# Optimization experiments

Hardware: AMD Instinct MI355X
Metric: run time of the kernel (lower is better)

The kernel has to match this reference:

```python
import jax, jax.numpy as jnp
import numpy as np

T, H = 4096, 2048

def setup_inputs() -> dict:
    key = jax.random.key(0)
    k1, k2, k3 = jax.random.split(key, 3)
    x_sequence = jax.random.normal(k1, (T, H), dtype=jnp.float32)
    lamda = jax.random.normal(k2, (H,), dtype=jnp.float32) * 0.2
    B = jax.random.normal(k3, (H, H), dtype=jnp.float32) / jnp.sqrt(jnp.float32(H))
    return {"x_sequence": x_sequence, "lamda": lamda, "B": B}

def reference(x_sequence, lamda, B):
    # h_t = lamda \odot h_{t-1} + B @ x_t ; initial h_0 = 0 (reset_rtrl_state).
    # Returns stacked h over all T steps, matching torch.stack(outputs).
    def step(h, x_t):
        h_next = lamda * h + B @ x_t  # [H]
        return h_next, h_next
    h0 = jnp.zeros_like(lamda)
    _, hs = jax.lax.scan(step, h0, x_sequence)  # hs: [T, H]
    return hs
```

## Files before the change

kernel.cpp:

```cpp
#include <hip/hip_runtime.h>
#include <hip/hip_bf16.h>

#define T_DIM 4096
#define H_DIM 2048
#define K_DIM 2048
#define NCHUNK 64
#define CLEN 64
#define NT (K_DIM / 64)

typedef float f32x4 __attribute__((ext_vector_type(4)));
typedef _Float16 f16x8 __attribute__((ext_vector_type(8)));

typedef const __attribute__((address_space(1))) char* gp1;
typedef __attribute__((address_space(3))) char* lp3;

static const size_t nX = (size_t)T_DIM * K_DIM;
static const size_t nB = (size_t)H_DIM * K_DIM;

__global__ __launch_bounds__(256) void cvt_swz_all(const float* __restrict__ X,
                                                   const float* __restrict__ Bm,
                                                   _Float16* __restrict__ Xh,
                                                   _Float16* __restrict__ Bh) {
    size_t i = ((size_t)blockIdx.x * 256 + threadIdx.x) * 8;
    const float* in;
    _Float16* out;
    size_t j;
    if (i < nX) { in = X;  out = Xh; j = i; }
    else        { in = Bm; out = Bh; j = i - nX; }
    int row  = (int)(j >> 11);
    int colB = (int)(j & 2047) * 2;
    float a[8];
    *(f32x4*)(a)     = *(const f32x4*)(in + j);
    *(f32x4*)(a + 4) = *(const f32x4*)(in + j + 4);
    f16x8 h;
#pragma unroll
    for (int k = 0; k < 8; ++k) h[k] = (_Float16)a[k];
    size_t ob = (size_t)row * 4096 + (size_t)(colB ^ ((row & 7) << 4));
    *(f16x8*)((char*)out + ob) = h;
}

__global__ __launch_bounds__(256) void gemm_f16(const _Float16* __restrict__ Xh,
                                                const _Float16* __restrict__ Bh,
                                                const float* __restrict__ lamda,
                                                float* __restrict__ Y,
                                                float* __restrict__ e) {
    __shared__ __align__(16) _Float16 sA[2][128 * 64];
    __shared__ __align__(16) _Float16 sB[2][128 * 64];

    int bid = blockIdx.x;
    int swz = (bid & 7) * 64 + (bid >> 3);
    const int h0 = (swz & 15) * 128;
    const int t0 = (swz >> 4) * 128;

    const int tid  = threadIdx.x;
    const int lane = tid & 63;
    const int wave = tid >> 6;
    const int wrow = wave >> 1;
    const int wcol = wave & 1;
    const int ln15 = lane & 15;
    const int kq   = lane >> 4;

    f32x4 acc[4][4] = {};

    const int srow = tid >> 3;
    const int kcB  = (tid & 7) * 16;
    size_t gA0[4], gB0[4];
    unsigned ldsOff[4];
#pragma unroll
    for (int t = 0; t < 4; ++t) {
        gA0[t] = (size_t)(t0 + srow + t * 32) * 4096 + kcB;
        gB0[t] = (size_t)(h0 + srow + t * 32) * 4096 + kcB;
        ldsOff[t] = (unsigned)((t * 256 + wave * 64) * 16);
    }

    int baseA[4], swzA[4], baseB[4], swzB[4];
#pragma unroll
    for (int m = 0; m < 4; ++m) {
        int rA = wrow * 64 + m * 16 + ln15;
        baseA[m] = rA * 128; swzA[m] = (rA & 7) << 4;
        int rB = wcol * 64 + m * 16 + ln15;
        baseB[m] = rB * 128; swzB[m] = (rB & 7) << 4;
    }

#define STAGE(buf, kt)                                                                   \
    {                                                                                    \
        _Pragma("unroll")                                                                \
        for (int t = 0; t < 4; ++t) {                                                    \
            __builtin_amdgcn_global_load_lds((gp1)((const char*)Xh + gA0[t] + (kt) * 128), \
                                             (lp3)((char*)sA[buf] + ldsOff[t]), 16, 0, 0); \
            __builtin_amdgcn_global_load_lds((gp1)((const char*)Bh + gB0[t] + (kt) * 128), \
                                             (lp3)((char*)sB[buf] + ldsOff[t]), 16, 0, 0); \
        }                                                                                \
    }

#define COMPUTE(buf)                                                                     \
    {                                                                                    \
        const char* pA = (const char*)sA[buf];                                           \
        const char* pB = (const char*)sB[buf];                                           \
        _Pragma("unroll")                                                                \
        for (int kk = 0; kk < 2; ++kk) {                                                 \
            const int kb = kk * 64 + kq * 16;                                            \
            f16x8 fa[4], fb[4];                                                          \
            _Pragma("unroll")                                                            \
            for (int m = 0; m < 4; ++m)                                                  \
                fa[m] = *(const f16x8*)(pA + baseA[m] + (kb ^ swzA[m]));                 \
            _Pragma("unroll")                                                            \
            for (int m = 0; m < 4; ++m)                                                  \
                fb[m] = *(const f16x8*)(pB + baseB[m] + (kb ^ swzB[m]));                 \
            _Pragma("unroll")                                                            \
            for (int m = 0; m < 4; ++m)                                                  \
                _Pragma("unroll")                                                        \
                for (int n = 0; n < 4; ++n)                                              \
                    acc[m][n] = __builtin_amdgcn_mfma_f32_16x16x32_f16(fa[m], fb[n],     \
                                                                      acc[m][n], 0, 0, 0); \
        }                                                                                \
    }

    STAGE(0, 0);
    int cur = 0;
    for (int kt = 0; kt < NT - 1; ++kt) {
        STAGE(cur ^ 1, kt + 1);
        asm volatile("s_waitcnt vmcnt(8)" ::: "memory");
        __builtin_amdgcn_sched_barrier(0);
        __builtin_amdgcn_s_barrier();
        __builtin_amdgcn_sched_barrier(0);
        COMPUTE(cur);
        __builtin_amdgcn_sched_barrier(0);
        asm volatile("s_waitcnt lgkmcnt(0)" ::: "memory");
        __builtin_amdgcn_s_barrier();
        __builtin_amdgcn_sched_barrier(0);
        cur ^= 1;
    }
    asm volatile("s_waitcnt vmcnt(0)" ::: "memory");
    __builtin_amdgcn_sched_barrier(0);
    __builtin_amdgcn_s_barrier();
    __builtin_amdgcn_sched_barrier(0);
    COMPUTE(cur);
#undef STAGE
#undef COMPUTE

#pragma unroll
    for (int m = 0; m < 4; ++m) {
        int row = t0 + wrow * 64 + m * 16 + kq * 4;
#pragma unroll
        for (int n = 0; n < 4; ++n) {
            int col = h0 + wcol * 64 + n * 16 + ln15;
#pragma unroll
            for (int j = 0; j < 4; ++j)
                Y[(size_t)(row + j) * H_DIM + col] = acc[m][n][j];
        }
    }

    const int c = (t0 >> 6) + wrow;
#pragma unroll
    for (int n = 0; n < 4; ++n) {
        int col = h0 + wcol * 64 + n * 16 + ln15;
        float lam  = lamda[col];
        float lam2 = lam * lam;
        float lam4 = lam2 * lam2;
        float lam16 = lam4 * lam4 * lam4 * lam4;
        float hsum = 0.f;
#pragma unroll
        for (int m = 0; m < 4; ++m) {
            float hm = fmaf(fmaf(fmaf(acc[m][n][0], lam, acc[m][n][1]), lam,
                                 acc[m][n][2]), lam, acc[m][n][3]);
            hsum = fmaf(hsum, lam16, hm);
        }
        float w = 1.f;
        if (kq < 3) w = lam4;
        if (kq < 2) w *= lam4;
        if (kq < 1) w *= lam4;
        float T = hsum * w;
        T += __shfl_xor(T, 16);
        T += __shfl_xor(T, 32);
        if (kq == 0) e[(size_t)c * H_DIM + col] = T;
    }
}

__global__ __launch_bounds__(256) void scanCB(float* __restrict__ Y,
                                              const float* __restrict__ lamda,
                                              const float* __restrict__ e) {
    int c = blockIdx.x >> 3;
    int h = (blockIdx.x & 7) * 256 + threadIdx.x;
    float lam = lamda[h];
    float lamL = lam;
#pragma unroll
    for (int i = 0; i < 6; ++i) lamL *= lamL;
    float s = 0.f;
    for (int ci = 0; ci < c; ++ci)
        s = fmaf(lamL, s, e[(size_t)ci * H_DIM + h]);
    float* q = Y + (size_t)c * CLEN * H_DIM + h;
#pragma unroll
    for (int t = 0; t < CLEN; ++t) {
        float v = fmaf(lam, s, q[(size_t)t * H_DIM]);
        q[(size_t)t * H_DIM] = v;
        s = v;
    }
}

__global__ __launch_bounds__(256) void gemm_xbT_split(const float* __restrict__ X,
                                                      const float* __restrict__ Bm,
                                                      float* __restrict__ Y) {
    __shared__ __align__(16) _Float16 Ah[128 * 64];
    __shared__ __align__(16) _Float16 Al[128 * 64];
    __shared__ __align__(16) _Float16 Bh2[128 * 64];
    __shared__ __align__(16) _Float16 Bl[128 * 64];

    const int tid  = threadIdx.x;
    const int t0   = blockIdx.y * 128;
    const int h0   = blockIdx.x * 128;
    const int lane = tid & 63;
    const int wave = tid >> 6;
    const int wrow = wave >> 1;
    const int wcol = wave & 1;
    const int ln15 = lane & 15;
    const int kq   = lane >> 4;

    f32x4 acc[4][4] = {};

    int baseA[4], swzA[4], baseB[4], swzB[4];
#pragma unroll
    for (int m = 0; m < 4; ++m) {
        int rA = wrow * 64 + m * 16 + ln15;
        baseA[m] = rA * 128; swzA[m] = (rA & 7) << 4;
        int rB = wcol * 64 + m * 16 + ln15;
        baseB[m] = rB * 128; swzB[m] = (rB & 7) << 4;
    }

    for (int kt = 0; kt < NT; ++kt) {
        const int k0 = kt * 64;
        __syncthreads();
#pragma unroll
        for (int t = 0; t < 4; ++t) {
            int c   = tid + t * 256;
            int row = c >> 3;
            int kc  = (c & 7) * 8;
            size_t gA = (size_t)(t0 + row) * K_DIM + k0 + kc;
            size_t gB = (size_t)(h0 + row) * K_DIM + k0 + kc;
            float a[8], b[8];
            *(float4*)(a)     = *(const float4*)(X + gA);
            *(float4*)(a + 4) = *(const float4*)(X + gA + 4);
            *(float4*)(b)     = *(const float4*)(Bm + gB);
            *(float4*)(b + 4) = *(const float4*)(Bm + gB + 4);
            f16x8 ah, al, bh, bl;
#pragma unroll
            for (int j = 0; j < 8; ++j) {
                _Float16 hh = (_Float16)a[j];
                ah[j] = hh; al[j] = (_Float16)(a[j] - (float)hh);
                _Float16 gg = (_Float16)b[j];
                bh[j] = gg; bl[j] = (_Float16)(b[j] - (float)gg);
            }
            int off = row * 128 + ((kc * 2) ^ ((row & 7) << 4));
            *(f16x8*)((char*)Ah + off)  = ah;
            *(f16x8*)((char*)Al + off)  = al;
            *(f16x8*)((char*)Bh2 + off) = bh;
            *(f16x8*)((char*)Bl + off)  = bl;
        }
        __syncthreads();
#pragma unroll
        for (int kk = 0; kk < 2; ++kk) {
            const int kb = kk * 64 + kq * 16;
            f16x8 fa[4], fb[4], ft[4];
#pragma unroll
            for (int m = 0; m < 4; ++m)
                fa[m] = *(const f16x8*)((const char*)Ah + baseA[m] + (kb ^ swzA[m]));
#pragma unroll
            for (int m = 0; m < 4; ++m)
                fb[m] = *(const f16x8*)((const char*)Bh2 + baseB[m] + (kb ^ swzB[m]));
#pragma unroll
            for (int m = 0; m < 4; ++m)
#pragma unroll
                for (int n = 0; n < 4; ++n)
                    acc[m][n] = __builtin_amdgcn_mfma_f32_16x16x32_f16(fa[m], fb[n], acc[m][n], 0, 0, 0);
#pragma unroll
            for (int m = 0; m < 4; ++m)
                ft[m] = *(const f16x8*)((const char*)Bl + baseB[m] + (kb ^ swzB[m]));
#pragma unroll
            for (int m = 0; m < 4; ++m)
#pragma unroll
                for (int n = 0; n < 4; ++n)
                    acc[m][n] = __builtin_amdgcn_mfma_f32_16x16x32_f16(fa[m], ft[n], acc[m][n], 0, 0, 0);
#pragma unroll
            for (int m = 0; m < 4; ++m)
                ft[m] = *(const f16x8*)((const char*)Al + baseA[m] + (kb ^ swzA[m]));
#pragma unroll
            for (int m = 0; m < 4; ++m)
#pragma unroll
                for (int n = 0; n < 4; ++n)
                    acc[m][n] = __builtin_amdgcn_mfma_f32_16x16x32_f16(ft[m], fb[n], acc[m][n], 0, 0, 0);
        }
    }

#pragma unroll
    for (int m = 0; m < 4; ++m) {
        int row = t0 + wrow * 64 + m * 16 + kq * 4;
#pragma unroll
        for (int n = 0; n < 4; ++n) {
            int col = h0 + wcol * 64 + n * 16 + ln15;
#pragma unroll
            for (int j = 0; j < 4; ++j)
                Y[(size_t)(row + j) * H_DIM + col] = acc[m][n][j];
        }
    }
}

__global__ __launch_bounds__(256) void scanA(const float* __restrict__ Y,
                                             const float* __restrict__ lamda,
                                             float* __restrict__ e) {
    int c = blockIdx.x >> 3;
    int h = (blockIdx.x & 7) * 256 + threadIdx.x;
    float lam = lamda[h];
    float s = 0.f;
    const float* p = Y + (size_t)c * CLEN * H_DIM + h;
#pragma unroll
    for (int t = 0; t < CLEN; ++t) { s = fmaf(lam, s, *p); p += H_DIM; }
    e[(size_t)c * H_DIM + h] = s;
}

extern "C" void kernel_launch(void* const* d_in, const int* in_sizes, int n_in,
                              void* d_out, int out_size, void* d_ws, size_t ws_size,
                              hipStream_t stream) {
    const float* X   = (const float*)d_in[0];
    const float* lam = (const float*)d_in[1];
    const float* Bm  = (const float*)d_in[2];
    float* Y = (float*)d_out;

    const size_t needFused = (nX + nB) * sizeof(_Float16)
                           + (size_t)NCHUNK * H_DIM * sizeof(float);

    if (ws_size >= needFused) {
        _Float16* Xh = (_Float16*)d_ws;
        _Float16* Bh = Xh + nX;
        float* e = (float*)(Bh + nB);

        int cvtBlocks = (int)((nX + nB) / 8 / 256);
        cvt_swz_all<<<dim3(cvtBlocks), 256, 0, stream>>>(X, Bm, Xh, Bh);
        gemm_f16<<<dim3(512), 256, 0, stream>>>(Xh, Bh, lam, Y, e);
        scanCB<<<dim3(NCHUNK * 8), 256, 0, stream>>>(Y, lam, e);
    } else {
        dim3 grid(H_DIM / 128, T_DIM / 128);
        gemm_xbT_split<<<grid, 256, 0, stream>>>(X, Bm, Y);
        float* e = (float*)d_ws;
        scanA<<<dim3(NCHUNK * 8), 256, 0, stream>>>(Y, lam, e);
        scanCB<<<dim3(NCHUNK * 8), 256, 0, stream>>>(Y, lam, e);
    }
}
```

Baseline: 81.91 us.

## Use 512-thread GEMM blocks with 8 waves and simplify the pipeline barriers

The fp16 GEMM block grows from 4 to 8 waves in a 2x4 layout. Each wave now computes a 64x32 sub-tile, so it holds fewer accumulators and each thread issues half as many global-to-LDS loads per stage. The hand-tuned vmcnt waits and sched_barrier fences are replaced by plain __syncthreads, and the loop absorbs the tail compute. The aim is more waves per CU to hide latency, at the cost of lower per-wave register reuse (more LDS reads per MFMA) and coarser synchronisation.

Result: faster. 77.23 us (-5.7%).

```diff
diff --git a/kernel.cpp b/kernel.cpp
--- a/kernel.cpp
+++ b/kernel.cpp
@@ -39,7 +39,7 @@
     *(f16x8*)((char*)out + ob) = h;
 }
 
-__global__ __launch_bounds__(256) void gemm_f16(const _Float16* __restrict__ Xh,
+__global__ __launch_bounds__(512) void gemm_f16(const _Float16* __restrict__ Xh,
                                                 const _Float16* __restrict__ Bh,
                                                 const float* __restrict__ lamda,
                                                 float* __restrict__ Y,
@@ -55,41 +55,44 @@
     const int tid  = threadIdx.x;
     const int lane = tid & 63;
     const int wave = tid >> 6;
-    const int wrow = wave >> 1;
-    const int wcol = wave & 1;
+    const int wrow = wave >> 2;
+    const int wcol = wave & 3;
     const int ln15 = lane & 15;
     const int kq   = lane >> 4;
 
-    f32x4 acc[4][4] = {};
+    f32x4 acc[4][2] = {};
 
     const int srow = tid >> 3;
     const int kcB  = (tid & 7) * 16;
-    size_t gA0[4], gB0[4];
-    unsigned ldsOff[4];
-#pragma unroll
-    for (int t = 0; t < 4; ++t) {
-        gA0[t] = (size_t)(t0 + srow + t * 32) * 4096 + kcB;
-        gB0[t] = (size_t)(h0 + srow + t * 32) * 4096 + kcB;
-        ldsOff[t] = (unsigned)((t * 256 + wave * 64) * 16);
-    }
-
-    int baseA[4], swzA[4], baseB[4], swzB[4];
+    size_t gA0[2], gB0[2];
+    unsigned ldsOff[2];
+#pragma unroll
+    for (int q = 0; q < 2; ++q) {
+        gA0[q] = (size_t)(t0 + srow + q * 64) * 4096 + kcB;
+        gB0[q] = (size_t)(h0 + srow + q * 64) * 4096 + kcB;
+        ldsOff[q] = (unsigned)((q * 512 + wave * 64) * 16);
+    }
+
+    int baseA[4], swzA[4], baseB[2], swzB[2];
 #pragma unroll
     for (int m = 0; m < 4; ++m) {
         int rA = wrow * 64 + m * 16 + ln15;
         baseA[m] = rA * 128; swzA[m] = (rA & 7) << 4;
-        int rB = wcol * 64 + m * 16 + ln15;
-        baseB[m] = rB * 128; swzB[m] = (rB & 7) << 4;
+    }
+#pragma unroll
+    for (int n = 0; n < 2; ++n) {
+        int rB = wcol * 32 + n * 16 + ln15;
+        baseB[n] = rB * 128; swzB[n] = (rB & 7) << 4;
     }
 
 #define STAGE(buf, kt)                                                                   \
     {                                                                                    \
         _Pragma("unroll")                                                                \
-        for (int t = 0; t < 4; ++t) {                                                    \
-            __builtin_amdgcn_global_load_lds((gp1)((const char*)Xh + gA0[t] + (kt) * 128), \
-                                             (lp3)((char*)sA[buf] + ldsOff[t]), 16, 0, 0); \
-            __builtin_amdgcn_global_load_lds((gp1)((const char*)Bh + gB0[t] + (kt) * 128), \
-                                             (lp3)((char*)sB[buf] + ldsOff[t]), 16, 0, 0); \
+        for (int q = 0; q < 2; ++q) {                                                    \
+            __builtin_amdgcn_global_load_lds((gp1)((const char*)Xh + gA0[q] + (kt) * 128), \
+                                             (lp3)((char*)sA[buf] + ldsOff[q]), 16, 0, 0); \
+            __builtin_amdgcn_global_load_lds((gp1)((const char*)Bh + gB0[q] + (kt) * 128), \
+                                             (lp3)((char*)sB[buf] + ldsOff[q]), 16, 0, 0); \
         }                                                                                \
     }
 
@@ -100,42 +103,32 @@
         _Pragma("unroll")                                                                \
         for (int kk = 0; kk < 2; ++kk) {                                                 \
             const int kb = kk * 64 + kq * 16;                                            \
-            f16x8 fa[4], fb[4];                                                          \
+            f16x8 fa[4], fb[2];                                                          \
             _Pragma("unroll")                                                            \
             for (int m = 0; m < 4; ++m)                                                  \
                 fa[m] = *(const f16x8*)(pA + baseA[m] + (kb ^ swzA[m]));                 \
             _Pragma("unroll")                                                            \
-            for (int m = 0; m < 4; ++m)                                                  \
-                fb[m] = *(const f16x8*)(pB + baseB[m] + (kb ^ swzB[m]));                 \
+            for (int n = 0; n < 2; ++n)                                                  \
+                fb[n] = *(const f16x8*)(pB + baseB[n] + (kb ^ swzB[n]));                 \
             _Pragma("unroll")                                                            \
             for (int m = 0; m < 4; ++m)                                                  \
                 _Pragma("unroll")                                                        \
-                for (int n = 0; n < 4; ++n)                                              \
+                for (int n = 0; n < 2; ++n)                                              \
                     acc[m][n] = __builtin_amdgcn_mfma_f32_16x16x32_f16(fa[m], fb[n],     \
                                                                       acc[m][n], 0, 0, 0); \
         }                                                                                \
     }
 
     STAGE(0, 0);
+    __syncthreads();
+
     int cur = 0;
-    for (int kt = 0; kt < NT - 1; ++kt) {
-        STAGE(cur ^ 1, kt + 1);
-        asm volatile("s_waitcnt vmcnt(8)" ::: "memory");
-        __builtin_amdgcn_sched_barrier(0);
-        __builtin_amdgcn_s_barrier();
-        __builtin_amdgcn_sched_barrier(0);
+    for (int kt = 0; kt < NT; ++kt) {
+        if (kt + 1 < NT) STAGE(cur ^ 1, kt + 1);
         COMPUTE(cur);
-        __builtin_amdgcn_sched_barrier(0);
-        asm volatile("s_waitcnt lgkmcnt(0)" ::: "memory");
-        __builtin_amdgcn_s_barrier();
-        __builtin_amdgcn_sched_barrier(0);
+        __syncthreads();
         cur ^= 1;
     }
-    asm volatile("s_waitcnt vmcnt(0)" ::: "memory");
-    __builtin_amdgcn_sched_barrier(0);
-    __builtin_amdgcn_s_barrier();
-    __builtin_amdgcn_sched_barrier(0);
-    COMPUTE(cur);
 #undef STAGE
 #undef COMPUTE
 
@@ -143,8 +136,8 @@
     for (int m = 0; m < 4; ++m) {
         int row = t0 + wrow * 64 + m * 16 + kq * 4;
 #pragma unroll
-        for (int n = 0; n < 4; ++n) {
-            int col = h0 + wcol * 64 + n * 16 + ln15;
+        for (int n = 0; n < 2; ++n) {
+            int col = h0 + wcol * 32 + n * 16 + ln15;
 #pragma unroll
             for (int j = 0; j < 4; ++j)
                 Y[(size_t)(row + j) * H_DIM + col] = acc[m][n][j];
@@ -153,8 +146,8 @@
 
     const int c = (t0 >> 6) + wrow;
 #pragma unroll
-    for (int n = 0; n < 4; ++n) {
-        int col = h0 + wcol * 64 + n * 16 + ln15;
+    for (int n = 0; n < 2; ++n) {
+        int col = h0 + wcol * 32 + n * 16 + ln15;
         float lam  = lamda[col];
         float lam2 = lam * lam;
         float lam4 = lam2 * lam2;
@@ -335,7 +328,7 @@
 
         int cvtBlocks = (int)((nX + nB) / 8 / 256);
         cvt_swz_all<<<dim3(cvtBlocks), 256, 0, stream>>>(X, Bm, Xh, Bh);
-        gemm_f16<<<dim3(512), 256, 0, stream>>>(Xh, Bh, lam, Y, e);
+        gemm_f16<<<dim3(512), 512, 0, stream>>>(Xh, Bh, lam, Y, e);
         scanCB<<<dim3(NCHUNK * 8), 256, 0, stream>>>(Y, lam, e);
     } else {
         dim3 grid(H_DIM / 128, T_DIM / 128);
```
